# Optimization experiments

Hardware: AMD Instinct MI355X
Metric: run time of the kernel (lower is better)

Reference implementation:

```python
import jax, jax.numpy as jnp
import numpy as np

BATCH = 2048
DIMS = [256, 256, 256, 128]  # input, hidden, hidden, output
N_ATOMS = 4  # identity, sin, tanh, square


def setup_inputs() -> dict:
    key = jax.random.key(0)
    ks = jax.random.split(key, 8)
    inp = {"x": jax.random.normal(ks[0], (BATCH, DIMS[0]), dtype=jnp.float32)}
    for li in range(3):
        out_d, in_d = DIMS[li + 1], DIMS[li]
        inp[f"W{li}"] = jax.random.normal(ks[1 + li], (out_d, in_d), dtype=jnp.float32) * 0.1
        inp[f"b{li}"] = jnp.zeros((out_d,), dtype=jnp.float32)
        inp[f"f_idx{li}"] = jax.random.randint(ks[4 + li], (out_d, in_d), 0, N_ATOMS, dtype=jnp.int32)
    return inp


def _w_eff(W, idx):
    # per-element atom nonlinearity selected by idx: [identity, sin, tanh, square]
    atoms = jnp.stack([W, jnp.sin(W), jnp.tanh(W), W * W], axis=0)  # [A, out, in]
    return jnp.take_along_axis(atoms, idx[None].astype(jnp.int32), axis=0)[0]


def reference(x, W0, b0, W1, b1, W2, b2, f_idx0, f_idx1, f_idx2):
    layers = [(W0, b0, f_idx0), (W1, b1, f_idx1), (W2, b2, f_idx2)]
    h = x
    n = len(layers)
    for li, (W, b, idx) in enumerate(layers):
        We = _w_eff(W, idx)                       # [out, in]
        z = h[:, None, :] * We[None, :, :]        # [batch, out, in]
        gz = z if li == n - 1 else jnp.tanh(z)    # g_fixed='tanh' on hidden layers
        h = gz.sum(axis=-1) + b[None, :]          # [batch, out]
    return h
```

## Files before the change

kernel.cpp:

```cpp
#include <hip/hip_runtime.h>
#include <math.h>


#define RB 4

__device__ __forceinline__ float fast_rcp(float x)  { return __builtin_amdgcn_rcpf(x); }
__device__ __forceinline__ float fast_exp2(float x) { return __builtin_amdgcn_exp2f(x); }

__global__ void weff_kernel(const float* __restrict__ W0, const int* __restrict__ I0,
                            const float* __restrict__ W1, const int* __restrict__ I1,
                            const float* __restrict__ W2, const int* __restrict__ I2,
                            float* __restrict__ ws) {
    int tid = blockIdx.x * blockDim.x + threadIdx.x;
    const float* W; const int* I; float* out; int outd; int e;
    if (tid < 65536)        { W = W0; I = I0; out = ws;          outd = 256; e = tid; }
    else if (tid < 131072)  { W = W1; I = I1; out = ws + 65536;  outd = 256; e = tid - 65536; }
    else if (tid < 163840)  { W = W2; I = I2; out = ws + 131072; outd = 128; e = tid - 131072; }
    else return;
    int o = e >> 8;
    int i = e & 255;
    float w = W[e];
    int idx = I[e];
    float v = w;
    if (idx == 1) v = sinf(w);
    else if (idx == 2) v = tanhf(w);
    else if (idx == 3) v = w * w;
    out[i * outd + o] = v;
}

__global__ __launch_bounds__(256) void mlp_kernel(
    const float* __restrict__ x,  const float* __restrict__ b0,
    const float* __restrict__ b1, const float* __restrict__ b2,
    const float* __restrict__ ws, float* __restrict__ out) {
    const float* We0 = ws;
    const float* We1 = ws + 65536;
    const float* We2 = ws + 131072;

    __shared__ __align__(16) float hA[RB][256];
    __shared__ __align__(16) float hB[RB][256];

    const int t = threadIdx.x;
    const int row0 = blockIdx.x * RB;
    const float SC  = 2.885390081777927f;
    const float INV = 1.0f / 2.885390081777927f;

#pragma unroll
    for (int k = 0; k < RB; k++)
        hA[k][t] = x[(row0 + k) * 256 + t] * SC;
    __syncthreads();

    {
        const float bias = b0[t];
        float acc[RB];
#pragma unroll
        for (int r = 0; r < RB; r++) acc[r] = 0.f;
        for (int i = 0; i < 256; i += 4) {
            float w0 = We0[(i + 0) * 256 + t];
            float w1 = We0[(i + 1) * 256 + t];
            float w2 = We0[(i + 2) * 256 + t];
            float w3 = We0[(i + 3) * 256 + t];
#pragma unroll
            for (int r = 0; r < RB; r++) {
                float4 h4 = *(const float4*)&hA[r][i];
                acc[r] += fast_rcp(fast_exp2(h4.x * w0) + 1.f);
                acc[r] += fast_rcp(fast_exp2(h4.y * w1) + 1.f);
                acc[r] += fast_rcp(fast_exp2(h4.z * w2) + 1.f);
                acc[r] += fast_rcp(fast_exp2(h4.w * w3) + 1.f);
            }
        }
#pragma unroll
        for (int r = 0; r < RB; r++)
            hB[r][t] = (256.0f - 2.0f * acc[r] + bias) * SC;
        __syncthreads();
    }

    {
        const float bias = b1[t];
        float acc[RB];
#pragma unroll
        for (int r = 0; r < RB; r++) acc[r] = 0.f;
        for (int i = 0; i < 256; i += 4) {
            float w0 = We1[(i + 0) * 256 + t];
            float w1 = We1[(i + 1) * 256 + t];
            float w2 = We1[(i + 2) * 256 + t];
            float w3 = We1[(i + 3) * 256 + t];
#pragma unroll
            for (int r = 0; r < RB; r++) {
                float4 h4 = *(const float4*)&hB[r][i];
                acc[r] += fast_rcp(fast_exp2(h4.x * w0) + 1.f);
                acc[r] += fast_rcp(fast_exp2(h4.y * w1) + 1.f);
                acc[r] += fast_rcp(fast_exp2(h4.z * w2) + 1.f);
                acc[r] += fast_rcp(fast_exp2(h4.w * w3) + 1.f);
            }
        }
#pragma unroll
        for (int r = 0; r < RB; r++)
            hA[r][t] = (256.0f - 2.0f * acc[r] + bias) * SC;
        __syncthreads();
    }

    {
        const int o  = t & 127;
        const int rg = t >> 7;
        const float bias = b2[o];
        float acc0 = 0.f, acc1 = 0.f;
        for (int i = 0; i < 256; i += 4) {
            float w0 = We2[(i + 0) * 128 + o];
            float w1 = We2[(i + 1) * 128 + o];
            float w2 = We2[(i + 2) * 128 + o];
            float w3 = We2[(i + 3) * 128 + o];
            {
                float4 h4 = *(const float4*)&hA[rg * 2 + 0][i];
                acc0 += h4.x * w0 + h4.y * w1 + h4.z * w2 + h4.w * w3;
            }
            {
                float4 h4 = *(const float4*)&hA[rg * 2 + 1][i];
                acc1 += h4.x * w0 + h4.y * w1 + h4.z * w2 + h4.w * w3;
            }
        }
        out[(row0 + rg * 2 + 0) * 128 + o] = acc0 * INV + bias;
        out[(row0 + rg * 2 + 1) * 128 + o] = acc1 * INV + bias;
    }
}

extern "C" void kernel_launch(void* const* d_in, const int* in_sizes, int n_in,
                              void* d_out, int out_size, void* d_ws, size_t ws_size,
                              hipStream_t stream) {
    const float* x  = (const float*)d_in[0];
    const float* W0 = (const float*)d_in[1];
    const float* b0 = (const float*)d_in[2];
    const int*   I0 = (const int*)  d_in[3];
    const float* W1 = (const float*)d_in[4];
    const float* b1 = (const float*)d_in[5];
    const int*   I1 = (const int*)  d_in[6];
    const float* W2 = (const float*)d_in[7];
    const float* b2 = (const float*)d_in[8];
    const int*   I2 = (const int*)  d_in[9];
    float* ws  = (float*)d_ws;
    float* out = (float*)d_out;

    weff_kernel<<<640, 256, 0, stream>>>(W0, I0, W1, I1, W2, I2, ws);
    mlp_kernel<<<2048 / RB, 256, 0, stream>>>(x, b0, b1, b2, ws, out);
}
```

Measured before the change: 140.3 us.

## Interleave effective weights for float4 loads, halve rows per block, use fast atom math

The weight-prep kernel now stores effective weights in a layout that interleaves groups of four input indices, so the MLP kernel can fetch four weights with a single float4 load. Rows per block drop from four to two, which doubles the grid to 1024 blocks to raise occupancy, at the cost of reusing each weight load across fewer rows. The prep kernel also replaces the branched sinf and tanhf calls with hardware sin and exp2/rcp approximations, computing all atoms and then selecting one, which may lose some accuracy.

```diff
diff --git a/kernel.cpp b/kernel.cpp
--- a/kernel.cpp
+++ b/kernel.cpp
@@ -2,10 +2,14 @@
 #include <math.h>
 
 
-#define RB 4
+#define RB 2
 
 __device__ __forceinline__ float fast_rcp(float x)  { return __builtin_amdgcn_rcpf(x); }
 __device__ __forceinline__ float fast_exp2(float x) { return __builtin_amdgcn_exp2f(x); }
+
+#define SC  2.885390081777927f
+#define INV (1.0f / 2.885390081777927f)
+#define INV2PI 0.15915494309189535f
 
 __global__ void weff_kernel(const float* __restrict__ W0, const int* __restrict__ I0,
                             const float* __restrict__ W1, const int* __restrict__ I1,
@@ -21,28 +25,26 @@
     int i = e & 255;
     float w = W[e];
     int idx = I[e];
-    float v = w;
-    if (idx == 1) v = sinf(w);
-    else if (idx == 2) v = tanhf(w);
-    else if (idx == 3) v = w * w;
-    out[i * outd + o] = v;
+    float sn = __builtin_amdgcn_sinf(w * INV2PI);
+    float th = 1.0f - 2.0f * fast_rcp(fast_exp2(w * SC) + 1.0f);
+    float sq = w * w;
+    float v = (idx == 1) ? sn : (idx == 2) ? th : (idx == 3) ? sq : w;
+    out[(i >> 2) * (outd * 4) + o * 4 + (i & 3)] = v;
 }
 
 __global__ __launch_bounds__(256) void mlp_kernel(
     const float* __restrict__ x,  const float* __restrict__ b0,
     const float* __restrict__ b1, const float* __restrict__ b2,
     const float* __restrict__ ws, float* __restrict__ out) {
-    const float* We0 = ws;
-    const float* We1 = ws + 65536;
-    const float* We2 = ws + 131072;
+    const float4* We0 = (const float4*)ws;
+    const float4* We1 = (const float4*)(ws + 65536);
+    const float4* We2 = (const float4*)(ws + 131072);
 
     __shared__ __align__(16) float hA[RB][256];
     __shared__ __align__(16) float hB[RB][256];
 
     const int t = threadIdx.x;
     const int row0 = blockIdx.x * RB;
-    const float SC  = 2.885390081777927f;
-    const float INV = 1.0f / 2.885390081777927f;
 
 #pragma unroll
     for (int k = 0; k < RB; k++)
@@ -51,75 +53,59 @@
 
     {
         const float bias = b0[t];
-        float acc[RB];
-#pragma unroll
-        for (int r = 0; r < RB; r++) acc[r] = 0.f;
-        for (int i = 0; i < 256; i += 4) {
-            float w0 = We0[(i + 0) * 256 + t];
-            float w1 = We0[(i + 1) * 256 + t];
-            float w2 = We0[(i + 2) * 256 + t];
-            float w3 = We0[(i + 3) * 256 + t];
-#pragma unroll
-            for (int r = 0; r < RB; r++) {
-                float4 h4 = *(const float4*)&hA[r][i];
-                acc[r] += fast_rcp(fast_exp2(h4.x * w0) + 1.f);
-                acc[r] += fast_rcp(fast_exp2(h4.y * w1) + 1.f);
-                acc[r] += fast_rcp(fast_exp2(h4.z * w2) + 1.f);
-                acc[r] += fast_rcp(fast_exp2(h4.w * w3) + 1.f);
-            }
+        float acc0 = 0.f, acc1 = 0.f;
+#pragma unroll 4
+        for (int ic = 0; ic < 64; ic++) {
+            float4 w  = We0[ic * 256 + t];
+            float4 h0 = *(const float4*)&hA[0][ic * 4];
+            float4 h1 = *(const float4*)&hA[1][ic * 4];
+            acc0 += fast_rcp(fast_exp2(h0.x * w.x) + 1.f);
+            acc0 += fast_rcp(fast_exp2(h0.y * w.y) + 1.f);
+            acc0 += fast_rcp(fast_exp2(h0.z * w.z) + 1.f);
+            acc0 += fast_rcp(fast_exp2(h0.w * w.w) + 1.f);
+            acc1 += fast_rcp(fast_exp2(h1.x * w.x) + 1.f);
+            acc1 += fast_rcp(fast_exp2(h1.y * w.y) + 1.f);
+            acc1 += fast_rcp(fast_exp2(h1.z * w.z) + 1.f);
+            acc1 += fast_rcp(fast_exp2(h1.w * w.w) + 1.f);
         }
-#pragma unroll
-        for (int r = 0; r < RB; r++)
-            hB[r][t] = (256.0f - 2.0f * acc[r] + bias) * SC;
+        hB[0][t] = (256.0f - 2.0f * acc0 + bias) * SC;
+        hB[1][t] = (256.0f - 2.0f * acc1 + bias) * SC;
         __syncthreads();
     }
 
     {
         const float bias = b1[t];
-        float acc[RB];
-#pragma unroll
-        for (int r = 0; r < RB; r++) acc[r] = 0.f;
-        for (int i = 0; i < 256; i += 4) {
-            float w0 = We1[(i + 0) * 256 + t];
-            float w1 = We1[(i + 1) * 256 + t];
-            float w2 = We1[(i + 2) * 256 + t];
-            float w3 = We1[(i + 3) * 256 + t];
-#pragma unroll
-            for (int r = 0; r < RB; r++) {
-                float4 h4 = *(const float4*)&hB[r][i];
-                acc[r] += fast_rcp(fast_exp2(h4.x * w0) + 1.f);
-                acc[r] += fast_rcp(fast_exp2(h4.y * w1) + 1.f);
-                acc[r] += fast_rcp(fast_exp2(h4.z * w2) + 1.f);
-                acc[r] += fast_rcp(fast_exp2(h4.w * w3) + 1.f);
-            }
+        float acc0 = 0.f, acc1 = 0.f;
+#pragma unroll 4
+        for (int ic = 0; ic < 64; ic++) {
+            float4 w  = We1[ic * 256 + t];
+            float4 h0 = *(const float4*)&hB[0][ic * 4];
+            float4 h1 = *(const float4*)&hB[1][ic * 4];
+            acc0 += fast_rcp(fast_exp2(h0.x * w.x) + 1.f);
+            acc0 += fast_rcp(fast_exp2(h0.y * w.y) + 1.f);
+            acc0 += fast_rcp(fast_exp2(h0.z * w.z) + 1.f);
+            acc0 += fast_rcp(fast_exp2(h0.w * w.w) + 1.f);
+            acc1 += fast_rcp(fast_exp2(h1.x * w.x) + 1.f);
+            acc1 += fast_rcp(fast_exp2(h1.y * w.y) + 1.f);
+            acc1 += fast_rcp(fast_exp2(h1.z * w.z) + 1.f);
+            acc1 += fast_rcp(fast_exp2(h1.w * w.w) + 1.f);
         }
-#pragma unroll
-        for (int r = 0; r < RB; r++)
-            hA[r][t] = (256.0f - 2.0f * acc[r] + bias) * SC;
+        hA[0][t] = (256.0f - 2.0f * acc0 + bias) * SC;
+        hA[1][t] = (256.0f - 2.0f * acc1 + bias) * SC;
         __syncthreads();
     }
 
     {
-        const int o  = t & 127;
-        const int rg = t >> 7;
-        const float bias = b2[o];
-        float acc0 = 0.f, acc1 = 0.f;
-        for (int i = 0; i < 256; i += 4) {
-            float w0 = We2[(i + 0) * 128 + o];
-            float w1 = We2[(i + 1) * 128 + o];
-            float w2 = We2[(i + 2) * 128 + o];
-            float w3 = We2[(i + 3) * 128 + o];
-            {
-                float4 h4 = *(const float4*)&hA[rg * 2 + 0][i];
-                acc0 += h4.x * w0 + h4.y * w1 + h4.z * w2 + h4.w * w3;
-            }
-            {
-                float4 h4 = *(const float4*)&hA[rg * 2 + 1][i];
-                acc1 += h4.x * w0 + h4.y * w1 + h4.z * w2 + h4.w * w3;
-            }
+        const int o = t & 127;
+        const int r = t >> 7;
+        float acc = 0.f;
+#pragma unroll 4
+        for (int ic = 0; ic < 64; ic++) {
+            float4 w = We2[ic * 128 + o];
+            float4 h = *(const float4*)&hA[r][ic * 4];
+            acc += h.x * w.x + h.y * w.y + h.z * w.z + h.w * w.w;
         }
-        out[(row0 + rg * 2 + 0) * 128 + o] = acc0 * INV + bias;
-        out[(row0 + rg * 2 + 1) * 128 + o] = acc1 * INV + bias;
+        out[(row0 + r) * 128 + o] = acc * INV + b2[o];
     }
 }
 
```

After: 130.0 us. 1.08x faster.
